# Kernel tuning notes

Measured on AMD Instinct MI355X. Metric: run time of the kernel, lower is better.

The kernel has to match this reference:

```python
import jax, jax.numpy as jnp
import numpy as np

EMBEDDING_DIM = 256
NUM_EMBEDDINGS = 8192
COMMITMENT_COST = 0.25
DECAY = 0.99
EPSILON = 1e-5


def setup_inputs() -> dict:
    key = jax.random.key(0)
    k1, k2 = jax.random.split(key)
    inputs = jax.random.normal(k1, (16, 32, 32, EMBEDDING_DIM), dtype=jnp.float32)
    # VarianceScaling(distribution='uniform'), fan_in scaling over [D, K]
    limit = float(np.sqrt(3.0 / EMBEDDING_DIM))
    embeddings = jax.random.uniform(k2, (EMBEDDING_DIM, NUM_EMBEDDINGS),
                                    minval=-limit, maxval=limit, dtype=jnp.float32)
    return {
        'inputs': inputs,
        'embeddings': embeddings,
        'ema_cs_hidden': jnp.zeros((NUM_EMBEDDINGS,), jnp.float32),
        'ema_dw_hidden': embeddings,  # hk initializes ema_dw to the embeddings
        'counter': 0,
        'is_training': 1,
    }


def reference(inputs, embeddings, ema_cs_hidden, ema_dw_hidden, counter, is_training):
    flat = inputs.reshape(-1, EMBEDDING_DIM)                        # [N, D]
    distances = (jnp.sum(flat ** 2, axis=1, keepdims=True)
                 - 2.0 * (flat @ embeddings)
                 + jnp.sum(embeddings ** 2, axis=0, keepdims=True))  # [N, K]
    encoding_indices = jnp.argmax(-distances, axis=1)                # [N]
    encodings = jax.nn.one_hot(encoding_indices, NUM_EMBEDDINGS,
                               dtype=distances.dtype)                # [N, K]
    idx = encoding_indices.reshape(inputs.shape[:-1])
    quantized = embeddings.T[idx]                                    # gather codebook
    e_latent_loss = jnp.mean((jax.lax.stop_gradient(quantized) - inputs) ** 2)
    loss = COMMITMENT_COST * e_latent_loss

    if is_training:
        # haiku ExponentialMovingAverage with zero-debias
        new_counter = counter + 1
        debias = 1.0 - DECAY ** new_counter
        cs_hidden = ema_cs_hidden * DECAY + jnp.sum(encodings, axis=0) * (1.0 - DECAY)
        cs_avg = cs_hidden / debias                                  # [K]
        dw = flat.T @ encodings                                      # [D, K] scatter-add as GEMM
        dw_hidden = ema_dw_hidden * DECAY + dw * (1.0 - DECAY)
        dw_avg = dw_hidden / debias
        n = jnp.sum(cs_avg)
        cs_norm = (cs_avg + EPSILON) / (n + NUM_EMBEDDINGS * EPSILON) * n
        new_embeddings = dw_avg / cs_norm[None, :]                   # [D, K]
    else:
        new_embeddings = embeddings

    # straight-through estimator
    quantized_st = inputs + jax.lax.stop_gradient(quantized - inputs)
    avg_probs = jnp.mean(encodings, axis=0)
    perplexity = jnp.exp(-jnp.sum(avg_probs * jnp.log(avg_probs + 1e-10)))
    return (quantized_st, loss, perplexity, idx, new_embeddings)
```

## Files before the change

kernel.cpp:

```cpp
#include <hip/hip_runtime.h>
#include <math.h>

#define DD 256
#define KK 8192
#define NN 16384
#define DECAYF 0.99f
#define EPSF 1e-5f
#define TAU 4e-3f

#define O_Q    0
#define O_LOSS 4194304
#define O_PERP 4194305
#define O_IDX  4194306
#define O_EMB  4210690

typedef float f32x4 __attribute__((ext_vector_type(4)));
typedef _Float16 f16x8 __attribute__((ext_vector_type(8)));

__device__ __forceinline__ unsigned short f2h(float f) {
  union { _Float16 h; unsigned short u; } c;
  c.h = (_Float16)f;
  return c.u;
}

__device__ __forceinline__ void gll16(const void* g, void* l) {
  __builtin_amdgcn_global_load_lds((const __attribute__((address_space(1))) void*)g,
                                   (__attribute__((address_space(3))) void*)l, 16, 0, 0);
}

#define DPPI(x, ctrl) __builtin_amdgcn_update_dpp((x), (x), (ctrl), 0xf, 0xf, true)
#define DPPF(x, ctrl) __int_as_float(__builtin_amdgcn_update_dpp(__float_as_int(x), __float_as_int(x), (ctrl), 0xf, 0xf, true))

__global__ void k_convert_xe(const float* __restrict__ x, unsigned short* __restrict__ Ah,
                             const float* __restrict__ emb, unsigned short* __restrict__ Eh,
                             float* __restrict__ embT, float* __restrict__ esqp,
                             unsigned long long* __restrict__ keysR,
                             float* __restrict__ counts, float* __restrict__ loss_part,
                             int* __restrict__ listc) {
  __shared__ float ld[32 * 33];
  int bx = blockIdx.x;
  int t = threadIdx.x;
  if (bx < 4096) {
    int i = bx * 256 + t;
    float4 v = ((const float4*)x)[i];
    ushort4 h;
    h.x = f2h(v.x); h.y = f2h(v.y); h.z = f2h(v.z); h.w = f2h(v.w);
    ((ushort4*)Ah)[i] = h;
    if (bx < 64) {
      keysR[bx * 256 + t] = ~0ull;
    } else if (bx < 96) {
      counts[(bx - 64) * 256 + t] = 0.f;
    } else if (bx == 96) {
      loss_part[t] = 0.f;
      if (t == 0) *listc = 0;
    }
    return;
  }
  int eb = bx - 4096;
  int k0 = (eb & 255) * 32, d0b = eb >> 8;
  {
    int din = t >> 3, kq = (t & 7) * 4;
    float4 v = *(const float4*)(emb + (size_t)(d0b * 32 + din) * KK + k0 + kq);
    ld[din * 33 + kq + 0] = v.x; ld[din * 33 + kq + 1] = v.y;
    ld[din * 33 + kq + 2] = v.z; ld[din * 33 + kq + 3] = v.w;
  }
  __syncthreads();
  int kout = t >> 3, dq = (t & 7) * 4;
  float f0 = ld[(dq + 0) * 33 + kout], f1 = ld[(dq + 1) * 33 + kout];
  float f2 = ld[(dq + 2) * 33 + kout], f3 = ld[(dq + 3) * 33 + kout];
  size_t o = (size_t)(k0 + kout) * DD + d0b * 32 + dq;
  float4 fv; fv.x = f0; fv.y = f1; fv.z = f2; fv.w = f3;
  *(float4*)(embT + o) = fv;
  ushort4 hv;
  hv.x = f2h(f0); hv.y = f2h(f1); hv.z = f2h(f2); hv.w = f2h(f3);
  *(ushort4*)(Eh + o) = hv;
  float p = (f0 * f0 + f1 * f1) + (f2 * f2 + f3 * f3);
  p += __shfl_xor(p, 1, 64);
  p += __shfl_xor(p, 2, 64);
  p += __shfl_xor(p, 4, 64);
  if ((t & 7) == 0) esqp[(size_t)(k0 + kout) * 8 + d0b] = p;
}

__launch_bounds__(256, 2)
__global__ void k_dist_mfma(const unsigned short* __restrict__ Ah, const unsigned short* __restrict__ Bh,
                            const float* __restrict__ esqp,
                            float* __restrict__ part1, float* __restrict__ part2,
                            int* __restrict__ partidx) {
  __shared__ __align__(16) unsigned short sB[8192];

  const int tid = threadIdx.x;
  const int w = tid >> 6, lane = tid & 63;
  const int kb = blockIdx.x, nb = blockIdx.y;
  const int row0 = nb * 128, col0 = kb * 128;
  const int m = lane & 15, q = lane >> 4;

  size_t gB[4];
  int lbB[4];
  #pragma unroll
  for (int s = 0; s < 4; ++s) {
    int g = w * 4 + s;
    int r = g * 8 + (lane >> 3);
    int c = (lane & 7) ^ (r & 7);
    gB[s] = (size_t)(col0 + r) * DD + c * 8;
    lbB[s] = g * 512;
  }

  const unsigned short* pA0 = Ah + (size_t)(row0 + w * 32 + m) * DD + q * 8;
  const unsigned short* pA1 = pA0 + 16 * DD;

  f32x4 acc[2][8];
  #pragma unroll
  for (int i = 0; i < 2; ++i)
    #pragma unroll
    for (int j = 0; j < 8; ++j) acc[i][j] = (f32x4)0.f;

  for (int it = 0; it < 4; ++it) {
    const int d0 = it * 64;
    __syncthreads();
    #pragma unroll
    for (int s = 0; s < 4; ++s) gll16(Bh + gB[s] + d0, sB + lbB[s]);
    f16x8 a[2][2];
    #pragma unroll
    for (int kk = 0; kk < 2; ++kk) {
      a[kk][0] = *(const f16x8*)(pA0 + d0 + kk * 32);
      a[kk][1] = *(const f16x8*)(pA1 + d0 + kk * 32);
    }
    __syncthreads();
    #pragma unroll
    for (int kk = 0; kk < 2; ++kk) {
      #pragma unroll
      for (int j = 0; j < 8; ++j) {
        int cn = j * 16 + m;
        int slot = (kk * 4 + q) ^ (cn & 7);
        f16x8 b = *(const f16x8*)(sB + cn * 64 + slot * 8);
        acc[0][j] = __builtin_amdgcn_mfma_f32_16x16x32_f16(a[kk][0], b, acc[0][j], 0, 0, 0);
        acc[1][j] = __builtin_amdgcn_mfma_f32_16x16x32_f16(a[kk][1], b, acc[1][j], 0, 0, 0);
      }
    }
  }

  float eq[8];
  #pragma unroll
  for (int j = 0; j < 8; ++j) {
    int cn = col0 + j * 16 + m;
    const float4* ep = (const float4*)esqp + cn * 2;
    float4 sa = ep[0], sb = ep[1];
    eq[j] = ((sa.x + sa.y) + (sa.z + sa.w)) + ((sb.x + sb.y) + (sb.z + sb.w));
  }

  #define RSTAGE(CTRL) {                                  \
    float ov = DPPF(m1, CTRL);                            \
    int   oi = DPPI(bi, CTRL);                            \
    float o2 = DPPF(m2, CTRL);                            \
    m2 = fminf(fminf(m2, o2), fmaxf(m1, ov));             \
    bool p = ov < m1;                                     \
    m1 = fminf(m1, ov);                                   \
    bi = p ? oi : bi;                                     \
  }
  #pragma unroll
  for (int i = 0; i < 2; ++i) {
    #pragma unroll
    for (int reg = 0; reg < 4; ++reg) {
      float m1 = 3.402823466e+38f, m2 = 3.402823466e+38f;
      int bi = 0;
      #pragma unroll
      for (int j = 0; j < 8; ++j) {
        float dd = fmaf(-2.0f, acc[i][j][reg], eq[j]);
        bool p = dd < m1;
        m2 = fminf(m2, fmaxf(dd, m1));
        m1 = fminf(m1, dd);
        bi = p ? (col0 + j * 16 + m) : bi;
      }
      RSTAGE(0xB1)
      RSTAGE(0x4E)
      RSTAGE(0x141)
      RSTAGE(0x140)
      if (m == 0) {
        int prow = row0 + w * 32 + i * 16 + q * 4 + reg;
        int pidx = prow * 64 + kb;
        part1[pidx] = m1; part2[pidx] = m2; partidx[pidx] = bi;
      }
    }
  }
  #undef RSTAGE
}

__global__ void k_argmin2(float* __restrict__ part1, float* __restrict__ part2,
                          const int* __restrict__ partidx, int* __restrict__ idxw,
                          int* __restrict__ listc, int* __restrict__ list) {
  int w = threadIdx.x >> 6, l = threadIdx.x & 63;
  int row = blockIdx.x * 4 + w;
  int f = blockIdx.x * 256 + threadIdx.x;
  float m1 = part1[f], m2 = part2[f];
  int bi = partidx[f];
  part1[f] = 0.f;
  part2[f] = 0.f;
  #pragma unroll
  for (int st = 1; st < 64; st <<= 1) {
    float ov = __shfl_xor(m1, st, 64);
    int   oi = __shfl_xor(bi, st, 64);
    float o2 = __shfl_xor(m2, st, 64);
    m2 = fminf(fminf(m2, o2), fmaxf(m1, ov));
    bool p = ov < m1;
    m1 = fminf(m1, ov);
    bi = p ? oi : bi;
  }
  if (l == 0) {
    idxw[row] = bi;
    if (m2 - m1 < TAU) { int pos = atomicAdd(listc, 1); list[pos] = row; }
  }
}

__global__ void k_rescore(const float* __restrict__ x, const float* __restrict__ emb,
                          const int* __restrict__ listc, const int* __restrict__ list,
                          unsigned long long* __restrict__ keysR) {
  __shared__ float se[8192];
  __shared__ double red[256];
  const int t = threadIdx.x;
  const int k0 = blockIdx.x * 32;
  int cnt = *listc;
  if ((int)blockIdx.y >= cnt) return;
  #pragma unroll
  for (int i = 0; i < 32; ++i) {
    int elem = i * 256 + t;
    int d = elem >> 5, c = elem & 31;
    se[d * 32 + c] = emb[(size_t)d * KK + k0 + c];
  }
  __syncthreads();
  const int c = t & 31, p = t >> 5;
  for (int li = blockIdx.y; li < cnt; li += gridDim.y) {
    int row = list[li];
    const float* xr = x + (size_t)row * DD;
    double acc = 0.0;
    #pragma unroll
    for (int j = 0; j < 32; ++j) {
      int d = p * 32 + j;
      double df = (double)xr[d] - (double)se[d * 32 + c];
      acc = fma(df, df, acc);
    }
    red[c * 8 + p] = acc;
    __syncthreads();
    if (t < 64) {
      unsigned long long key = ~0ull;
      if (t < 32) {
        double dist = 0.0;
        #pragma unroll
        for (int qq = 0; qq < 8; ++qq) dist += red[t * 8 + qq];
        key = ((unsigned long long)__double_as_longlong(dist) & ~0x1FFFull)
              | (unsigned long long)(k0 + t);
      }
      #pragma unroll
      for (int s = 1; s < 64; s <<= 1) {
        unsigned long long o = __shfl_xor(key, s, 64);
        if (o < key) key = o;
      }
      if (t == 0) atomicMin(&keysR[row], key);
    }
    __syncthreads();
  }
}

__global__ void k_gather(const float* __restrict__ x, const float* __restrict__ embT,
                         const int* __restrict__ idxw, const unsigned long long* __restrict__ keysR,
                         const int* __restrict__ train,
                         float* __restrict__ outq, float* __restrict__ outidx,
                         float* __restrict__ dwT, float* __restrict__ counts,
                         float* __restrict__ loss_part) {
  int w = threadIdx.x >> 6, l = threadIdx.x & 63;
  int n = blockIdx.x * 4 + w;
  unsigned long long kv = keysR[n];
  int k = (kv != ~0ull) ? (int)(kv & 0x1FFFull) : idxw[n];
  float4 xv = ((const float4*)(x + (size_t)n * DD))[l];
  float4 qv = ((const float4*)(embT + (size_t)k * DD))[l];
  int d = l * 4;

  ((float4*)(outq + (size_t)n * DD))[l] = qv;

  float e0 = qv.x - xv.x, e1 = qv.y - xv.y, e2 = qv.z - xv.z, e3 = qv.w - xv.w;
  float ls = (e0 * e0 + e1 * e1) + (e2 * e2 + e3 * e3);

  if (*train) {
    const float wdw = 1.0f - DECAYF;
    float* base = dwT + (size_t)k * DD + d;
    atomicAdd(base + 0, xv.x * wdw);
    atomicAdd(base + 1, xv.y * wdw);
    atomicAdd(base + 2, xv.z * wdw);
    atomicAdd(base + 3, xv.w * wdw);
  }

  #pragma unroll
  for (int s = 1; s < 64; s <<= 1) ls += __shfl_xor(ls, s, 64);
  if (l == 0) {
    atomicAdd(&loss_part[blockIdx.x & 255], ls);
    atomicAdd(&counts[k], 1.0f);
    outidx[n] = (float)k;
  }
}

__global__ void k_final(const float* __restrict__ dwT, const float* __restrict__ ema_dw,
                        const float* __restrict__ emb, const float* __restrict__ counts,
                        const float* __restrict__ ema_cs, const float* __restrict__ loss_part,
                        const int* __restrict__ counter, const int* __restrict__ train,
                        float* __restrict__ out4, float* __restrict__ outloss,
                        float* __restrict__ outperp) {
  __shared__ float ld[32 * 33];
  __shared__ float s_red[4], s_l[4], s_e[4];
  __shared__ float csn_s[32];
  int t = threadIdx.x;
  int k0 = blockIdx.x * 32, d0 = blockIdx.y * 32;
  int w = t >> 6, lane = t & 63;

  if (blockIdx.x == 0 && blockIdx.y == 0) {
    float lloc = loss_part[t];
    float eloc = 0.f;
    for (int i = 0; i < 32; ++i) {
      float cc = counts[t + i * 256];
      float pp = cc * (1.0f / 16384.0f);
      eloc += pp * logf(pp + 1e-10f);
    }
    #pragma unroll
    for (int s = 1; s < 64; s <<= 1) {
      lloc += __shfl_xor(lloc, s, 64);
      eloc += __shfl_xor(eloc, s, 64);
    }
    if (lane == 0) { s_l[w] = lloc; s_e[w] = eloc; }
    __syncthreads();
    if (t == 0) {
      outloss[0] = 0.25f * (((s_l[0] + s_l[1]) + (s_l[2] + s_l[3])) / 4194304.0f);
      outperp[0] = expf(-((s_e[0] + s_e[1]) + (s_e[2] + s_e[3])));
    }
  }

  if (*train) {
    float debias = 1.0f - powf(DECAYF, (float)(*counter + 1));
    float inv = 1.0f / debias;
    float nloc = 0.f;
    for (int i = 0; i < 32; ++i) {
      int k = t + i * 256;
      nloc += fmaf(counts[k], 1.0f - DECAYF, ema_cs[k] * DECAYF);
    }
    #pragma unroll
    for (int s = 1; s < 64; s <<= 1) nloc += __shfl_xor(nloc, s, 64);
    if (lane == 0) s_red[w] = nloc;
    __syncthreads();
    float nsum = ((s_red[0] + s_red[1]) + (s_red[2] + s_red[3])) * inv;
    if (t < 32) {
      int k = k0 + t;
      float a = fmaf(counts[k], 1.0f - DECAYF, ema_cs[k] * DECAYF) * inv;
      csn_s[t] = (a + EPSF) / (nsum + 8192.0f * EPSF) * nsum;
    }
    {
      int ki = t >> 3, dq = (t & 7) * 4;
      float4 v = *(const float4*)(dwT + (size_t)(k0 + ki) * DD + d0 + dq);
      ld[ki * 33 + dq + 0] = v.x; ld[ki * 33 + dq + 1] = v.y;
      ld[ki * 33 + dq + 2] = v.z; ld[ki * 33 + dq + 3] = v.w;
    }
    __syncthreads();
    int dout = t >> 3, kq = (t & 7) * 4;
    size_t o = (size_t)(d0 + dout) * KK + k0 + kq;
    float4 e = *(const float4*)(ema_dw + o);
    float4 r;
    r.x = fmaf(e.x, DECAYF, ld[(kq + 0) * 33 + dout]) * inv / csn_s[kq + 0];
    r.y = fmaf(e.y, DECAYF, ld[(kq + 1) * 33 + dout]) * inv / csn_s[kq + 1];
    r.z = fmaf(e.z, DECAYF, ld[(kq + 2) * 33 + dout]) * inv / csn_s[kq + 2];
    r.w = fmaf(e.w, DECAYF, ld[(kq + 3) * 33 + dout]) * inv / csn_s[kq + 3];
    *(float4*)(out4 + o) = r;
  } else {
    int dout = t >> 3, kq = (t & 7) * 4;
    size_t o = (size_t)(d0 + dout) * KK + k0 + kq;
    *(float4*)(out4 + o) = *(const float4*)(emb + o);
  }
}

extern "C" void kernel_launch(void* const* d_in, const int* in_sizes, int n_in,
                              void* d_out, int out_size, void* d_ws, size_t ws_size,
                              hipStream_t stream) {
  (void)in_sizes; (void)n_in; (void)out_size; (void)ws_size;
  const float* x      = (const float*)d_in[0];
  const float* emb    = (const float*)d_in[1];
  const float* ema_cs = (const float*)d_in[2];
  const float* ema_dw = (const float*)d_in[3];
  const int*   counter = (const int*)d_in[4];
  const int*   train   = (const int*)d_in[5];

  float* out = (float*)d_out;
  float* outq    = out + O_Q;
  float* outloss = out + O_LOSS;
  float* outperp = out + O_PERP;
  float* outidx  = out + O_IDX;
  float* out4    = out + O_EMB;

  char* W = (char*)d_ws;
  unsigned short* Ah   = (unsigned short*)(W);
  unsigned short* Eh   = (unsigned short*)(W + 8388608);
  float* embT          = (float*)(W + 12582912);
  float* part1         = (float*)(W + 20971520);
  float* part2         = (float*)(W + 25165824);
  int*   partidx       = (int*)(W + 29360128);
  float* dwT           = part1;
  unsigned long long* keysR = (unsigned long long*)(W + 33554432);
  float* esqp          = (float*)(W + 33685504);
  float* counts        = (float*)(W + 33947648);
  float* loss_part     = (float*)(W + 33980416);
  int*   listc         = (int*)(W + 33981440);
  int*   list          = (int*)(W + 33981444);
  int*   idxw          = (int*)(W + 34046980);

  k_convert_xe<<<6144, 256, 0, stream>>>(x, Ah, emb, Eh, embT, esqp, keysR, counts, loss_part, listc);
  k_dist_mfma<<<dim3(64, 128), 256, 0, stream>>>(Ah, Eh, esqp, part1, part2, partidx);
  k_argmin2<<<4096, 256, 0, stream>>>(part1, part2, partidx, idxw, listc, list);
  k_rescore<<<dim3(256, 8), 256, 0, stream>>>(x, emb, listc, list, keysR);
  k_gather<<<4096, 256, 0, stream>>>(x, embT, idxw, keysR, train, outq, outidx, dwT, counts, loss_part);
  k_final<<<dim3(256, 8), 256, 0, stream>>>(dwT, ema_dw, emb, counts, ema_cs, loss_part, counter, train, out4, outloss, outperp);
}
```

Before: 371.7 us.

## Fuse post-GEMM kernels into one persistent kernel with grid barriers

```diff
diff --git a/kernel.cpp b/kernel.cpp
--- a/kernel.cpp
+++ b/kernel.cpp
@@ -7,6 +7,7 @@
 #define DECAYF 0.99f
 #define EPSF 1e-5f
 #define TAU 4e-3f
+#define PBLK 512
 
 #define O_Q    0
 #define O_LOSS 4194304
@@ -30,6 +31,21 @@
 
 #define DPPI(x, ctrl) __builtin_amdgcn_update_dpp((x), (x), (ctrl), 0xf, 0xf, true)
 #define DPPF(x, ctrl) __int_as_float(__builtin_amdgcn_update_dpp(__float_as_int(x), __float_as_int(x), (ctrl), 0xf, 0xf, true))
+
+__device__ __forceinline__ void gbar(int* cnt, int* flag) {
+  __syncthreads();
+  if (threadIdx.x == 0) {
+    __threadfence();
+    if (atomicAdd(cnt, 1) == PBLK - 1) {
+      __threadfence();
+      atomicExch(flag, 1);
+    } else {
+      while (atomicAdd(flag, 0) == 0) __builtin_amdgcn_s_sleep(8);
+    }
+    __threadfence();
+  }
+  __syncthreads();
+}
 
 __global__ void k_convert_xe(const float* __restrict__ x, unsigned short* __restrict__ Ah,
                              const float* __restrict__ emb, unsigned short* __restrict__ Eh,
@@ -52,7 +68,7 @@
       counts[(bx - 64) * 256 + t] = 0.f;
     } else if (bx == 96) {
       loss_part[t] = 0.f;
-      if (t == 0) *listc = 0;
+      if (t < 7) listc[t] = 0;
     }
     return;
   }
@@ -87,12 +103,22 @@
                             float* __restrict__ part1, float* __restrict__ part2,
                             int* __restrict__ partidx) {
   __shared__ __align__(16) unsigned short sB[8192];
+  __shared__ float sEq[128];
 
   const int tid = threadIdx.x;
   const int w = tid >> 6, lane = tid & 63;
   const int kb = blockIdx.x, nb = blockIdx.y;
   const int row0 = nb * 128, col0 = kb * 128;
   const int m = lane & 15, q = lane >> 4;
+
+  {
+    int col = tid >> 1, half = tid & 1;
+    const float4* ep = (const float4*)esqp + (size_t)(col0 + col) * 2 + half;
+    float4 s = *ep;
+    float p = (s.x + s.y) + (s.z + s.w);
+    p += __shfl_xor(p, 1, 64);
+    if (half == 0) sEq[col] = p;
+  }
 
   size_t gB[4];
   int lbB[4];
@@ -141,12 +167,7 @@
 
   float eq[8];
   #pragma unroll
-  for (int j = 0; j < 8; ++j) {
-    int cn = col0 + j * 16 + m;
-    const float4* ep = (const float4*)esqp + cn * 2;
-    float4 sa = ep[0], sb = ep[1];
-    eq[j] = ((sa.x + sa.y) + (sa.z + sa.w)) + ((sb.x + sb.y) + (sb.z + sb.w));
-  }
+  for (int j = 0; j < 8; ++j) eq[j] = sEq[j * 16 + m];
 
   #define RSTAGE(CTRL) {                                  \
     float ov = DPPF(m1, CTRL);                            \
@@ -185,132 +206,137 @@
   #undef RSTAGE
 }
 
-__global__ void k_argmin2(float* __restrict__ part1, float* __restrict__ part2,
-                          const int* __restrict__ partidx, int* __restrict__ idxw,
-                          int* __restrict__ listc, int* __restrict__ list) {
-  int w = threadIdx.x >> 6, l = threadIdx.x & 63;
-  int row = blockIdx.x * 4 + w;
-  int f = blockIdx.x * 256 + threadIdx.x;
-  float m1 = part1[f], m2 = part2[f];
-  int bi = partidx[f];
-  part1[f] = 0.f;
-  part2[f] = 0.f;
-  #pragma unroll
-  for (int st = 1; st < 64; st <<= 1) {
-    float ov = __shfl_xor(m1, st, 64);
-    int   oi = __shfl_xor(bi, st, 64);
-    float o2 = __shfl_xor(m2, st, 64);
-    m2 = fminf(fminf(m2, o2), fmaxf(m1, ov));
-    bool p = ov < m1;
-    m1 = fminf(m1, ov);
-    bi = p ? oi : bi;
-  }
-  if (l == 0) {
-    idxw[row] = bi;
-    if (m2 - m1 < TAU) { int pos = atomicAdd(listc, 1); list[pos] = row; }
-  }
-}
-
-__global__ void k_rescore(const float* __restrict__ x, const float* __restrict__ emb,
-                          const int* __restrict__ listc, const int* __restrict__ list,
-                          unsigned long long* __restrict__ keysR) {
-  __shared__ float se[8192];
-  __shared__ double red[256];
+union SM {
+  struct { float se[8192]; double red[256]; } rs;
+  struct { float ld[32 * 33]; float s_red[4]; float s_l[4]; float s_e[4]; float csn[32]; } fi;
+};
+
+__launch_bounds__(256, 4)
+__global__ void k_post(float* __restrict__ part1, float* __restrict__ part2,
+                       const int* __restrict__ partidx, int* __restrict__ idxw,
+                       int* __restrict__ listc, int* __restrict__ list,
+                       const float* __restrict__ x, const float* __restrict__ emb,
+                       unsigned long long* __restrict__ keysR,
+                       const float* __restrict__ embT, const int* __restrict__ train,
+                       float* __restrict__ outq, float* __restrict__ outidx,
+                       float* __restrict__ dwT, float* __restrict__ counts,
+                       float* __restrict__ loss_part,
+                       const float* __restrict__ ema_dw, const float* __restrict__ ema_cs,
+                       const int* __restrict__ counter,
+                       float* __restrict__ out4, float* __restrict__ outloss,
+                       float* __restrict__ outperp, int* __restrict__ bar) {
+  __shared__ SM sm;
   const int t = threadIdx.x;
-  const int k0 = blockIdx.x * 32;
-  int cnt = *listc;
-  if ((int)blockIdx.y >= cnt) return;
-  #pragma unroll
-  for (int i = 0; i < 32; ++i) {
-    int elem = i * 256 + t;
-    int d = elem >> 5, c = elem & 31;
-    se[d * 32 + c] = emb[(size_t)d * KK + k0 + c];
-  }
-  __syncthreads();
-  const int c = t & 31, p = t >> 5;
-  for (int li = blockIdx.y; li < cnt; li += gridDim.y) {
-    int row = list[li];
-    const float* xr = x + (size_t)row * DD;
-    double acc = 0.0;
-    #pragma unroll
-    for (int j = 0; j < 32; ++j) {
-      int d = p * 32 + j;
-      double df = (double)xr[d] - (double)se[d * 32 + c];
-      acc = fma(df, df, acc);
-    }
-    red[c * 8 + p] = acc;
-    __syncthreads();
-    if (t < 64) {
-      unsigned long long key = ~0ull;
-      if (t < 32) {
-        double dist = 0.0;
+  const int w = t >> 6, l = t & 63;
+  const int tr = *train;
+
+  for (int it = 0; it < 8; ++it) {
+    int vb = blockIdx.x * 8 + it;
+    int row = vb * 4 + w;
+    int f = vb * 256 + t;
+    float m1 = part1[f], m2 = part2[f];
+    int bi = partidx[f];
+    part1[f] = 0.f;
+    part2[f] = 0.f;
+    #pragma unroll
+    for (int st = 1; st < 64; st <<= 1) {
+      float ov = __shfl_xor(m1, st, 64);
+      int   oi = __shfl_xor(bi, st, 64);
+      float o2 = __shfl_xor(m2, st, 64);
+      m2 = fminf(fminf(m2, o2), fmaxf(m1, ov));
+      bool p = ov < m1;
+      m1 = fminf(m1, ov);
+      bi = p ? oi : bi;
+    }
+    if (l == 0) {
+      idxw[row] = bi;
+      if (m2 - m1 < TAU) { int pos = atomicAdd(listc, 1); list[pos] = row; }
+    }
+  }
+  gbar(bar + 0, bar + 3);
+
+  {
+    int cnt = *listc;
+    for (int vb0 = 0; vb0 < 4; ++vb0) {
+      int vb = blockIdx.x * 4 + vb0;
+      int kslice = vb & 255, stripe = vb >> 8;
+      if (stripe < cnt) {
+        const int k0 = kslice * 32;
         #pragma unroll
-        for (int qq = 0; qq < 8; ++qq) dist += red[t * 8 + qq];
-        key = ((unsigned long long)__double_as_longlong(dist) & ~0x1FFFull)
-              | (unsigned long long)(k0 + t);
-      }
-      #pragma unroll
-      for (int s = 1; s < 64; s <<= 1) {
-        unsigned long long o = __shfl_xor(key, s, 64);
-        if (o < key) key = o;
-      }
-      if (t == 0) atomicMin(&keysR[row], key);
-    }
-    __syncthreads();
-  }
-}
-
-__global__ void k_gather(const float* __restrict__ x, const float* __restrict__ embT,
-                         const int* __restrict__ idxw, const unsigned long long* __restrict__ keysR,
-                         const int* __restrict__ train,
-                         float* __restrict__ outq, float* __restrict__ outidx,
-                         float* __restrict__ dwT, float* __restrict__ counts,
-                         float* __restrict__ loss_part) {
-  int w = threadIdx.x >> 6, l = threadIdx.x & 63;
-  int n = blockIdx.x * 4 + w;
-  unsigned long long kv = keysR[n];
-  int k = (kv != ~0ull) ? (int)(kv & 0x1FFFull) : idxw[n];
-  float4 xv = ((const float4*)(x + (size_t)n * DD))[l];
-  float4 qv = ((const float4*)(embT + (size_t)k * DD))[l];
-  int d = l * 4;
-
-  ((float4*)(outq + (size_t)n * DD))[l] = qv;
-
-  float e0 = qv.x - xv.x, e1 = qv.y - xv.y, e2 = qv.z - xv.z, e3 = qv.w - xv.w;
-  float ls = (e0 * e0 + e1 * e1) + (e2 * e2 + e3 * e3);
-
-  if (*train) {
-    const float wdw = 1.0f - DECAYF;
-    float* base = dwT + (size_t)k * DD + d;
-    atomicAdd(base + 0, xv.x * wdw);
-    atomicAdd(base + 1, xv.y * wdw);
-    atomicAdd(base + 2, xv.z * wdw);
-    atomicAdd(base + 3, xv.w * wdw);
-  }
-
-  #pragma unroll
-  for (int s = 1; s < 64; s <<= 1) ls += __shfl_xor(ls, s, 64);
-  if (l == 0) {
-    atomicAdd(&loss_part[blockIdx.x & 255], ls);
-    atomicAdd(&counts[k], 1.0f);
-    outidx[n] = (float)k;
-  }
-}
-
-__global__ void k_final(const float* __restrict__ dwT, const float* __restrict__ ema_dw,
-                        const float* __restrict__ emb, const float* __restrict__ counts,
-                        const float* __restrict__ ema_cs, const float* __restrict__ loss_part,
-                        const int* __restrict__ counter, const int* __restrict__ train,
-                        float* __restrict__ out4, float* __restrict__ outloss,
-                        float* __restrict__ outperp) {
-  __shared__ float ld[32 * 33];
-  __shared__ float s_red[4], s_l[4], s_e[4];
-  __shared__ float csn_s[32];
-  int t = threadIdx.x;
-  int k0 = blockIdx.x * 32, d0 = blockIdx.y * 32;
-  int w = t >> 6, lane = t & 63;
-
-  if (blockIdx.x == 0 && blockIdx.y == 0) {
+        for (int i = 0; i < 32; ++i) {
+          int elem = i * 256 + t;
+          int d = elem >> 5, c = elem & 31;
+          sm.rs.se[d * 32 + c] = emb[(size_t)d * KK + k0 + c];
+        }
+        __syncthreads();
+        const int c = t & 31, p = t >> 5;
+        for (int li = stripe; li < cnt; li += 8) {
+          int row = list[li];
+          const float* xr = x + (size_t)row * DD;
+          double acc = 0.0;
+          #pragma unroll
+          for (int j = 0; j < 32; ++j) {
+            int d = p * 32 + j;
+            double df = (double)xr[d] - (double)sm.rs.se[d * 32 + c];
+            acc = fma(df, df, acc);
+          }
+          sm.rs.red[c * 8 + p] = acc;
+          __syncthreads();
+          if (t < 64) {
+            unsigned long long key = ~0ull;
+            if (t < 32) {
+              double dist = 0.0;
+              #pragma unroll
+              for (int qq = 0; qq < 8; ++qq) dist += sm.rs.red[t * 8 + qq];
+              key = ((unsigned long long)__double_as_longlong(dist) & ~0x1FFFull)
+                    | (unsigned long long)(k0 + t);
+            }
+            #pragma unroll
+            for (int s = 1; s < 64; s <<= 1) {
+              unsigned long long o = __shfl_xor(key, s, 64);
+              if (o < key) key = o;
+            }
+            if (t == 0) atomicMin(&keysR[row], key);
+          }
+          __syncthreads();
+        }
+      }
+      __syncthreads();
+    }
+  }
+  gbar(bar + 1, bar + 4);
+
+  for (int it = 0; it < 8; ++it) {
+    int vb = blockIdx.x * 8 + it;
+    int n = vb * 4 + w;
+    unsigned long long kv = keysR[n];
+    int k = (kv != ~0ull) ? (int)(kv & 0x1FFFull) : idxw[n];
+    float4 xv = ((const float4*)(x + (size_t)n * DD))[l];
+    float4 qv = ((const float4*)(embT + (size_t)k * DD))[l];
+    int d = l * 4;
+    ((float4*)(outq + (size_t)n * DD))[l] = qv;
+    float e0 = qv.x - xv.x, e1 = qv.y - xv.y, e2 = qv.z - xv.z, e3 = qv.w - xv.w;
+    float ls = (e0 * e0 + e1 * e1) + (e2 * e2 + e3 * e3);
+    if (tr) {
+      const float wdw = 1.0f - DECAYF;
+      float* base = dwT + (size_t)k * DD + d;
+      atomicAdd(base + 0, xv.x * wdw);
+      atomicAdd(base + 1, xv.y * wdw);
+      atomicAdd(base + 2, xv.z * wdw);
+      atomicAdd(base + 3, xv.w * wdw);
+    }
+    #pragma unroll
+    for (int s = 1; s < 64; s <<= 1) ls += __shfl_xor(ls, s, 64);
+    if (l == 0) {
+      atomicAdd(&loss_part[vb & 255], ls);
+      atomicAdd(&counts[k], 1.0f);
+      outidx[n] = (float)k;
+    }
+  }
+  gbar(bar + 2, bar + 5);
+
+  float inv = 1.0f / (1.0f - powf(DECAYF, (float)(*counter + 1)));
+  if (blockIdx.x == 0) {
     float lloc = loss_part[t];
     float eloc = 0.f;
     for (int i = 0; i < 32; ++i) {
@@ -323,17 +349,16 @@
       lloc += __shfl_xor(lloc, s, 64);
       eloc += __shfl_xor(eloc, s, 64);
     }
-    if (lane == 0) { s_l[w] = lloc; s_e[w] = eloc; }
+    if (l == 0) { sm.fi.s_l[w] = lloc; sm.fi.s_e[w] = eloc; }
     __syncthreads();
     if (t == 0) {
-      outloss[0] = 0.25f * (((s_l[0] + s_l[1]) + (s_l[2] + s_l[3])) / 4194304.0f);
-      outperp[0] = expf(-((s_e[0] + s_e[1]) + (s_e[2] + s_e[3])));
-    }
-  }
-
-  if (*train) {
-    float debias = 1.0f - powf(DECAYF, (float)(*counter + 1));
-    float inv = 1.0f / debias;
+      outloss[0] = 0.25f * (((sm.fi.s_l[0] + sm.fi.s_l[1]) + (sm.fi.s_l[2] + sm.fi.s_l[3])) / 4194304.0f);
+      outperp[0] = expf(-((sm.fi.s_e[0] + sm.fi.s_e[1]) + (sm.fi.s_e[2] + sm.fi.s_e[3])));
+    }
+    __syncthreads();
+  }
+  float nsum = 0.f;
+  if (tr) {
     float nloc = 0.f;
     for (int i = 0; i < 32; ++i) {
       int k = t + i * 256;
@@ -341,34 +366,42 @@
     }
     #pragma unroll
     for (int s = 1; s < 64; s <<= 1) nloc += __shfl_xor(nloc, s, 64);
-    if (lane == 0) s_red[w] = nloc;
-    __syncthreads();
-    float nsum = ((s_red[0] + s_red[1]) + (s_red[2] + s_red[3])) * inv;
-    if (t < 32) {
-      int k = k0 + t;
-      float a = fmaf(counts[k], 1.0f - DECAYF, ema_cs[k] * DECAYF) * inv;
-      csn_s[t] = (a + EPSF) / (nsum + 8192.0f * EPSF) * nsum;
-    }
-    {
-      int ki = t >> 3, dq = (t & 7) * 4;
-      float4 v = *(const float4*)(dwT + (size_t)(k0 + ki) * DD + d0 + dq);
-      ld[ki * 33 + dq + 0] = v.x; ld[ki * 33 + dq + 1] = v.y;
-      ld[ki * 33 + dq + 2] = v.z; ld[ki * 33 + dq + 3] = v.w;
-    }
-    __syncthreads();
-    int dout = t >> 3, kq = (t & 7) * 4;
-    size_t o = (size_t)(d0 + dout) * KK + k0 + kq;
-    float4 e = *(const float4*)(ema_dw + o);
-    float4 r;
-    r.x = fmaf(e.x, DECAYF, ld[(kq + 0) * 33 + dout]) * inv / csn_s[kq + 0];
-    r.y = fmaf(e.y, DECAYF, ld[(kq + 1) * 33 + dout]) * inv / csn_s[kq + 1];
-    r.z = fmaf(e.z, DECAYF, ld[(kq + 2) * 33 + dout]) * inv / csn_s[kq + 2];
-    r.w = fmaf(e.w, DECAYF, ld[(kq + 3) * 33 + dout]) * inv / csn_s[kq + 3];
-    *(float4*)(out4 + o) = r;
-  } else {
-    int dout = t >> 3, kq = (t & 7) * 4;
-    size_t o = (size_t)(d0 + dout) * KK + k0 + kq;
-    *(float4*)(out4 + o) = *(const float4*)(emb + o);
+    if (l == 0) sm.fi.s_red[w] = nloc;
+    __syncthreads();
+    nsum = ((sm.fi.s_red[0] + sm.fi.s_red[1]) + (sm.fi.s_red[2] + sm.fi.s_red[3])) * inv;
+    __syncthreads();
+  }
+  for (int vb0 = 0; vb0 < 4; ++vb0) {
+    int vb = blockIdx.x * 4 + vb0;
+    int k0 = (vb & 255) * 32, d0 = (vb >> 8) * 32;
+    if (tr) {
+      if (t < 32) {
+        int k = k0 + t;
+        float a = fmaf(counts[k], 1.0f - DECAYF, ema_cs[k] * DECAYF) * inv;
+        sm.fi.csn[t] = (a + EPSF) / (nsum + 8192.0f * EPSF) * nsum;
+      }
+      {
+        int ki = t >> 3, dq = (t & 7) * 4;
+        float4 v = *(const float4*)(dwT + (size_t)(k0 + ki) * DD + d0 + dq);
+        sm.fi.ld[ki * 33 + dq + 0] = v.x; sm.fi.ld[ki * 33 + dq + 1] = v.y;
+        sm.fi.ld[ki * 33 + dq + 2] = v.z; sm.fi.ld[ki * 33 + dq + 3] = v.w;
+      }
+      __syncthreads();
+      int dout = t >> 3, kq = (t & 7) * 4;
+      size_t o = (size_t)(d0 + dout) * KK + k0 + kq;
+      float4 e = *(const float4*)(ema_dw + o);
+      float4 r;
+      r.x = fmaf(e.x, DECAYF, sm.fi.ld[(kq + 0) * 33 + dout]) * inv / sm.fi.csn[kq + 0];
+      r.y = fmaf(e.y, DECAYF, sm.fi.ld[(kq + 1) * 33 + dout]) * inv / sm.fi.csn[kq + 1];
+      r.z = fmaf(e.z, DECAYF, sm.fi.ld[(kq + 2) * 33 + dout]) * inv / sm.fi.csn[kq + 2];
+      r.w = fmaf(e.w, DECAYF, sm.fi.ld[(kq + 3) * 33 + dout]) * inv / sm.fi.csn[kq + 3];
+      *(float4*)(out4 + o) = r;
+      __syncthreads();
+    } else {
+      int dout = t >> 3, kq = (t & 7) * 4;
+      size_t o = (size_t)(d0 + dout) * KK + k0 + kq;
+      *(float4*)(out4 + o) = *(const float4*)(emb + o);
+    }
   }
 }
 
@@ -403,13 +436,14 @@
   float* counts        = (float*)(W + 33947648);
   float* loss_part     = (float*)(W + 33980416);
   int*   listc         = (int*)(W + 33981440);
-  int*   list          = (int*)(W + 33981444);
-  int*   idxw          = (int*)(W + 34046980);
+  int*   bar           = (int*)(W + 33981444);
+  int*   list          = (int*)(W + 33981504);
+  int*   idxw          = (int*)(W + 34047040);
 
   k_convert_xe<<<6144, 256, 0, stream>>>(x, Ah, emb, Eh, embT, esqp, keysR, counts, loss_part, listc);
   k_dist_mfma<<<dim3(64, 128), 256, 0, stream>>>(Ah, Eh, esqp, part1, part2, partidx);
-  k_argmin2<<<4096, 256, 0, stream>>>(part1, part2, partidx, idxw, listc, list);
-  k_rescore<<<dim3(256, 8), 256, 0, stream>>>(x, emb, listc, list, keysR);
-  k_gather<<<4096, 256, 0, stream>>>(x, embT, idxw, keysR, train, outq, outidx, dwT, counts, loss_part);
-  k_final<<<dim3(256, 8), 256, 0, stream>>>(dwT, ema_dw, emb, counts, ema_cs, loss_part, counter, train, out4, outloss, outperp);
-}
+  k_post<<<PBLK, 256, 0, stream>>>(part1, part2, partidx, idxw, listc, list,
+                                   x, emb, keysR, embT, train,
+                                   outq, outidx, dwT, counts, loss_part,
+                                   ema_dw, ema_cs, counter, out4, outloss, outperp, bar);
+}
```

After: 587.2 us. 57.9% more time.
